# Kernel optimization log

Hardware: AMD Instinct MI355X
Metric: run time of the kernel (lower is better)

Reference implementation:

```python
import jax, jax.numpy as jnp
import numpy as np

N = 100000      # nodes
E = 1600000     # edges (avg degree 16)
IN = 128        # input_dim
HID = 32        # hidden_dim per head (layer 1)
HEADS = 2       # heads (layer 1)
OUT = 32        # output_dim (layer 2, heads=1)
NEG_SLOPE = 0.2 # PyG GATConv default leaky relu slope


def setup_inputs() -> dict:
    key = jax.random.key(0)
    ks = jax.random.split(key, 10)
    s = 0.1  # glorot-ish scale
    x = jax.random.normal(ks[0], (N, IN), jnp.float32)
    edge_index = jax.random.randint(ks[1], (2, E), 0, N, dtype=jnp.int64)
    W1 = jax.random.normal(ks[2], (IN, HEADS * HID), jnp.float32) * s
    a1_src = jax.random.normal(ks[3], (HEADS, HID), jnp.float32) * s
    a1_dst = jax.random.normal(ks[4], (HEADS, HID), jnp.float32) * s
    b1 = jnp.zeros((HEADS * HID,), jnp.float32)
    W2 = jax.random.normal(ks[5], (HEADS * HID, OUT), jnp.float32) * s
    a2_src = jax.random.normal(ks[6], (1, OUT), jnp.float32) * s
    a2_dst = jax.random.normal(ks[7], (1, OUT), jnp.float32) * s
    b2 = jnp.zeros((OUT,), jnp.float32)
    return {"x": x, "edge_index": edge_index, "W1": W1, "a1_src": a1_src,
            "a1_dst": a1_dst, "b1": b1, "W2": W2, "a2_src": a2_src,
            "a2_dst": a2_dst, "b2": b2}


def _gat_layer(x, src, dst, W, a_src, a_dst, b, heads, out_ch, concat, n_nodes):
    # linear projection: [N, heads, out_ch]
    h = (x @ W).reshape(n_nodes, heads, out_ch)
    # per-node attention halves: [N, heads]
    alpha_s = jnp.einsum('nhc,hc->nh', h, a_src)
    alpha_d = jnp.einsum('nhc,hc->nh', h, a_dst)
    # per-edge raw score (message x_j = source node, softmax over dst segment)
    e = jax.nn.leaky_relu(alpha_s[src] + alpha_d[dst], NEG_SLOPE)  # [E, heads]
    # segment softmax over incoming edges of each dst node
    m = jax.ops.segment_max(e, dst, num_segments=n_nodes)          # [N, heads]
    m = jax.lax.stop_gradient(m)
    ee = jnp.exp(e - m[dst])
    denom = jax.ops.segment_sum(ee, dst, num_segments=n_nodes)     # [N, heads]
    alpha = ee / (denom[dst] + 1e-16)                              # [E, heads]
    # weighted scatter-add aggregation
    msg = h[src] * alpha[:, :, None]                               # [E, heads, out_ch]
    out = jax.ops.segment_sum(msg, dst, num_segments=n_nodes)      # [N, heads, out_ch]
    if concat:
        out = out.reshape(n_nodes, heads * out_ch)
    else:
        out = out.mean(axis=1)
    return out + b


def reference(x, edge_index, W1, a1_src, a1_dst, b1, W2, a2_src, a2_dst, b2):
    n = x.shape[0]
    # PyG GATConv adds self-loops by default (both layers, same edge set)
    loop = jnp.arange(n, dtype=edge_index.dtype)
    src = jnp.concatenate([edge_index[0], loop])
    dst = jnp.concatenate([edge_index[1], loop])
    h = _gat_layer(x, src, dst, W1, a1_src, a1_dst, b1, HEADS, HID, True, n)
    h = jax.nn.elu(h)
    return _gat_layer(h, src, dst, W2, a2_src, a2_dst, b2, 1, OUT, False, n)
```

## Files before the change

kernel.cpp:

```cpp
#include <hip/hip_runtime.h>
#include <math.h>

#define N_NODES 100000
#define N_EDGES 1600000
#define IN_DIM  128
#define C1      64
#define OUT_DIM 32
#define NEG_SLOPE 0.2f
#define LOG2E 1.44269504f

#define BSHIFT  8
#define BNODES  256
#define NBUCK   ((N_NODES + BNODES - 1) / BNODES)
#define CAP     5120
#define SLOTS   48
#define GC_STRIDE 16
#define G1_BLOCKS ((N_NODES + 127) / 128)
#define B1_BLOCKS ((N_EDGES + 4095) / 4096)

typedef _Float16 half8 __attribute__((ext_vector_type(8)));
typedef float    f32x4 __attribute__((ext_vector_type(4)));

__device__ __forceinline__ float wexp2(float sc) {
    return __builtin_amdgcn_exp2f(fmaxf(sc, NEG_SLOPE * sc));
}

__global__ void prep_k(const float* __restrict__ W1, const float* __restrict__ W2,
                       _Float16* __restrict__ w1t, _Float16* __restrict__ w2t,
                       int* __restrict__ gcur) {
    int t = blockIdx.x * 256 + threadIdx.x;
    if (t < NBUCK * GC_STRIDE) gcur[t] = 0;
    if (t < IN_DIM * C1) {
        int k = t >> 6, n = t & 63;
        w1t[n * IN_DIM + k] = (_Float16)W1[t];
    }
    if (t < C1 * OUT_DIM) {
        int k = t >> 5, n = t & 31;
        w2t[n * C1 + k] = (_Float16)W2[t];
    }
}

__global__ __launch_bounds__(256) void b1g1_k(const int* __restrict__ ei,
        int* __restrict__ gcur, int* __restrict__ buf,
        const float* __restrict__ x, const _Float16* __restrict__ w1t,
        const float* __restrict__ a_s, const float* __restrict__ a_d,
        _Float16* __restrict__ h, float* __restrict__ as_o,
        float* __restrict__ ad_o) {
    __shared__ __align__(16) char smem[4 * 32 * 72 * 2];
    int t = threadIdx.x;

    if (blockIdx.x < B1_BLOCKS) {
        int* scnt  = (int*)smem;
        int* sbase = scnt + NBUCK;
        int* soff  = sbase + NBUCK;
        for (int i = t; i < NBUCK; i += 256) { scnt[i] = 0; soff[i] = 0; }
        __syncthreads();
        int  s[16], bk[16], ld[16];
        bool v[16];
        #pragma unroll
        for (int i = 0; i < 16; ++i) {
            int e = blockIdx.x * 4096 + i * 256 + t;
            v[i] = e < N_EDGES;
            int ec = v[i] ? e : 0;
            s[i] = ei[ec];
            int d = ei[N_EDGES + ec];
            bk[i] = d >> BSHIFT;
            ld[i] = d & (BNODES - 1);
            if (v[i]) atomicAdd(&scnt[bk[i]], 1);
        }
        __syncthreads();
        for (int i = t; i < NBUCK; i += 256)
            sbase[i] = scnt[i] ? atomicAdd(&gcur[i * GC_STRIDE], scnt[i]) : 0;
        __syncthreads();
        #pragma unroll
        for (int i = 0; i < 16; ++i) {
            if (v[i]) {
                int p = sbase[bk[i]] + atomicAdd(&soff[bk[i]], 1);
                if (p < CAP) buf[bk[i] * CAP + p] = s[i] | (ld[i] << 17);
            }
        }
        return;
    }

    _Float16 (*sh)[32 * 72] = (_Float16(*)[32 * 72])smem;
    int wv = t >> 6, lane = t & 63, m = lane & 15, q = lane >> 4;
    int rbw = (blockIdx.x - B1_BLOCKS) * 128 + wv * 32;
    f32x4 acc[2][4];
    #pragma unroll
    for (int i = 0; i < 2; ++i)
        #pragma unroll
        for (int j = 0; j < 4; ++j) acc[i][j] = (f32x4){0.f, 0.f, 0.f, 0.f};
    #pragma unroll
    for (int ks = 0; ks < 4; ++ks) {
        half8 a[2];
        #pragma unroll
        for (int rt = 0; rt < 2; ++rt) {
            int r = rbw + rt * 16 + m;
            r = r < N_NODES ? r : 0;
            const float4* p = (const float4*)(x + (size_t)r * IN_DIM + ks * 32 + q * 8);
            float4 f0 = p[0], f1 = p[1];
            half8 av;
            av[0] = (_Float16)f0.x; av[1] = (_Float16)f0.y;
            av[2] = (_Float16)f0.z; av[3] = (_Float16)f0.w;
            av[4] = (_Float16)f1.x; av[5] = (_Float16)f1.y;
            av[6] = (_Float16)f1.z; av[7] = (_Float16)f1.w;
            a[rt] = av;
        }
        #pragma unroll
        for (int ct = 0; ct < 4; ++ct) {
            half8 b = *(const half8*)(w1t + (ct * 16 + m) * IN_DIM + ks * 32 + q * 8);
            acc[0][ct] = __builtin_amdgcn_mfma_f32_16x16x32_f16(a[0], b, acc[0][ct], 0, 0, 0);
            acc[1][ct] = __builtin_amdgcn_mfma_f32_16x16x32_f16(a[1], b, acc[1][ct], 0, 0, 0);
        }
    }
    _Float16* ws = sh[wv];
    #pragma unroll
    for (int rt = 0; rt < 2; ++rt)
        #pragma unroll
        for (int ct = 0; ct < 4; ++ct)
            #pragma unroll
            for (int r = 0; r < 4; ++r)
                ws[(rt * 16 + q * 4 + r) * 72 + ct * 16 + m] = (_Float16)acc[rt][ct][r];
    __syncthreads();
    int rl = lane >> 1, hp = lane & 1;
    int rg = rbw + rl;
    if (rg < N_NODES) {
        float As_r[32], Ad_r[32];
        const float4* ap = (const float4*)(a_s + hp * 32);
        const float4* dp = (const float4*)(a_d + hp * 32);
        #pragma unroll
        for (int i = 0; i < 8; ++i) {
            float4 v = ap[i];
            As_r[4*i] = v.x; As_r[4*i+1] = v.y; As_r[4*i+2] = v.z; As_r[4*i+3] = v.w;
            float4 u = dp[i];
            Ad_r[4*i] = u.x; Ad_r[4*i+1] = u.y; Ad_r[4*i+2] = u.z; Ad_r[4*i+3] = u.w;
        }
        const _Float16* rowp = ws + rl * 72 + hp * 32;
        half8 c0 = *(const half8*)(rowp);
        half8 c1 = *(const half8*)(rowp + 8);
        half8 c2 = *(const half8*)(rowp + 16);
        half8 c3 = *(const half8*)(rowp + 24);
        float s = 0.f, dd = 0.f;
        #pragma unroll
        for (int j = 0; j < 8; ++j) {
            s  = fmaf((float)c0[j], As_r[j],      s);
            dd = fmaf((float)c0[j], Ad_r[j],      dd);
            s  = fmaf((float)c1[j], As_r[8 + j],  s);
            dd = fmaf((float)c1[j], Ad_r[8 + j],  dd);
            s  = fmaf((float)c2[j], As_r[16 + j], s);
            dd = fmaf((float)c2[j], Ad_r[16 + j], dd);
            s  = fmaf((float)c3[j], As_r[24 + j], s);
            dd = fmaf((float)c3[j], Ad_r[24 + j], dd);
        }
        as_o[rg * 2 + hp] = s  * LOG2E;
        ad_o[rg * 2 + hp] = dd * LOG2E;
        _Float16* hr = h + (size_t)rg * C1 + hp * 32;
        *(half8*)(hr)      = c0;
        *(half8*)(hr + 8)  = c1;
        *(half8*)(hr + 16) = c2;
        *(half8*)(hr + 24) = c3;
    }
}

__global__ __launch_bounds__(256) void binp2_k(const int* __restrict__ gcur,
        const int* __restrict__ buf, int* __restrict__ csr, int* __restrict__ deg) {
    __shared__ int4 lcsr4[BNODES * SLOTS / 4];
    __shared__ int  lcnt[BNODES];
    int* lcsr = (int*)lcsr4;
    int b = blockIdx.x, t = threadIdx.x;
    lcnt[t] = 0;
    __syncthreads();
    int cnt = gcur[b * GC_STRIDE];
    if (cnt > CAP) cnt = CAP;
    const int* bb = buf + b * CAP;
    for (int e = t; e < cnt; e += 256) {
        int vv = bb[e];
        int src = vv & 0x1FFFF;
        int l = vv >> 17;
        int slot = atomicAdd(&lcnt[l], 1);
        if (slot < SLOTS) lcsr[l * SLOTS + slot] = src;
    }
    __syncthreads();
    int c = lcnt[t];
    int slot = c < SLOTS ? c : SLOTS - 1;
    lcsr[t * SLOTS + slot] = b * BNODES + t;
    int cd = c + 1;
    deg[b * BNODES + t] = cd < SLOTS ? cd : SLOTS;
    __syncthreads();
    int4* g4 = (int4*)csr + (size_t)b * (BNODES * SLOTS / 4);
    #pragma unroll
    for (int i = 0; i < BNODES * SLOTS / 4 / 256; ++i)
        g4[t + i * 256] = lcsr4[t + i * 256];
}

__global__ __launch_bounds__(256) void agg1g2_k(const int* __restrict__ deg,
        const int* __restrict__ csr, const _Float16* __restrict__ h1,
        const float* __restrict__ as1, const float* __restrict__ ad1,
        const float* __restrict__ b1, const _Float16* __restrict__ w2t,
        const float* __restrict__ a2s, const float* __restrict__ a2d,
        _Float16* __restrict__ h2, float* __restrict__ as2o,
        float* __restrict__ ad2o) {
    __shared__ int      srow[16 * SLOTS];
    __shared__ _Float16 shu[16 * 72];
    __shared__ _Float16 sh2[16 * 36];
    int t = threadIdx.x;
    int wv = t >> 6, lane = t & 63;
    int dl   = lane >> 4;
    int eg   = (lane >> 3) & 1;
    int cl   = lane & 7;
    int head = cl >> 2;
    int lr   = wv * 4 + dl;
    int d    = blockIdx.x * 16 + lr;

    if (t < 16 * SLOTS / 4)
        ((int4*)srow)[t] = ((const int4*)(csr + (size_t)blockIdx.x * 16 * SLOTS))[t];
    __syncthreads();

    int cnt = deg[d];
    const int* row = srow + lr * SLOTS;
    float advl = ad1[d * 2 + head];
    float acc[8] = {0.f, 0.f, 0.f, 0.f, 0.f, 0.f, 0.f, 0.f};
    float wsum = 0.f;
    for (int base = 0; base < cnt; base += 8) {
        int e0 = base + eg, e1 = e0 + 2, e2 = e0 + 4, e3 = e0 + 6;
        bool v0 = e0 < cnt, v1 = e1 < cnt, v2 = e2 < cnt, v3 = e3 < cnt;
        int s0 = row[v0 ? e0 : 0];
        int s1 = row[v1 ? e1 : 0];
        int s2 = row[v2 ? e2 : 0];
        int s3 = row[v3 ? e3 : 0];
        float a0 = as1[(unsigned)(s0 * 2 + head)];
        float a1 = as1[(unsigned)(s1 * 2 + head)];
        float a2 = as1[(unsigned)(s2 * 2 + head)];
        float a3 = as1[(unsigned)(s3 * 2 + head)];
        half8 g0 = *(const half8*)(h1 + (unsigned)(s0 * C1 + 8 * cl));
        half8 g1 = *(const half8*)(h1 + (unsigned)(s1 * C1 + 8 * cl));
        half8 g2 = *(const half8*)(h1 + (unsigned)(s2 * C1 + 8 * cl));
        half8 g3 = *(const half8*)(h1 + (unsigned)(s3 * C1 + 8 * cl));
        float w0 = v0 ? wexp2(a0 + advl) : 0.f;
        float w1 = v1 ? wexp2(a1 + advl) : 0.f;
        float w2 = v2 ? wexp2(a2 + advl) : 0.f;
        float w3 = v3 ? wexp2(a3 + advl) : 0.f;
        #pragma unroll
        for (int i = 0; i < 8; ++i) {
            acc[i] = fmaf((float)g0[i], w0, acc[i]);
            acc[i] = fmaf((float)g1[i], w1, acc[i]);
            acc[i] = fmaf((float)g2[i], w2, acc[i]);
            acc[i] = fmaf((float)g3[i], w3, acc[i]);
        }
        wsum += (w0 + w1) + (w2 + w3);
    }
    #pragma unroll
    for (int i = 0; i < 8; ++i) acc[i] += __shfl_xor(acc[i], 8);
    wsum += __shfl_xor(wsum, 8);
    if (eg == 0) {
        float inv = 1.f / (wsum + 1e-16f);
        const float4* bv = (const float4*)(b1 + 8 * cl);
        float o[8];
        #pragma unroll
        for (int i = 0; i < 4; ++i) {
            o[i]     = acc[i]     * inv + (&bv[0].x)[i];
            o[4 + i] = acc[4 + i] * inv + (&bv[1].x)[i];
        }
        half8 hv;
        #pragma unroll
        for (int i = 0; i < 8; ++i) {
            float e = o[i] > 0.f ? o[i] : __expf(o[i]) - 1.f;
            hv[i] = (_Float16)e;
        }
        *(half8*)(shu + lr * 72 + cl * 8) = hv;
    }
    __syncthreads();
    if (wv != 0) return;

    {
        int m = lane & 15, q = lane >> 4;
        f32x4 c2[2];
        c2[0] = (f32x4){0.f, 0.f, 0.f, 0.f};
        c2[1] = (f32x4){0.f, 0.f, 0.f, 0.f};
        #pragma unroll
        for (int ks = 0; ks < 2; ++ks) {
            half8 a = *(const half8*)(shu + m * 72 + ks * 32 + q * 8);
            #pragma unroll
            for (int ct = 0; ct < 2; ++ct) {
                half8 b = *(const half8*)(w2t + (ct * 16 + m) * C1 + ks * 32 + q * 8);
                c2[ct] = __builtin_amdgcn_mfma_f32_16x16x32_f16(a, b, c2[ct], 0, 0, 0);
            }
        }
        #pragma unroll
        for (int ct = 0; ct < 2; ++ct)
            #pragma unroll
            for (int r = 0; r < 4; ++r)
                sh2[(q * 4 + r) * 36 + ct * 16 + m] = (_Float16)c2[ct][r];
    }
    asm volatile("s_waitcnt lgkmcnt(0)" ::: "memory");
    __builtin_amdgcn_sched_barrier(0);

    {
        int r = lane & 15, p = lane >> 4;
        int rg = blockIdx.x * 16 + r;
        const float4* ap = (const float4*)(a2s + p * 8);
        const float4* dp = (const float4*)(a2d + p * 8);
        float4 av0 = ap[0], av1 = ap[1];
        float4 dv0 = dp[0], dv1 = dp[1];
        float As[8] = {av0.x, av0.y, av0.z, av0.w, av1.x, av1.y, av1.z, av1.w};
        float Ad[8] = {dv0.x, dv0.y, dv0.z, dv0.w, dv1.x, dv1.y, dv1.z, dv1.w};
        half8 c = *(const half8*)(sh2 + r * 36 + p * 8);
        float s = 0.f, dd = 0.f;
        #pragma unroll
        for (int j = 0; j < 8; ++j) {
            s  = fmaf((float)c[j], As[j], s);
            dd = fmaf((float)c[j], Ad[j], dd);
        }
        s  += __shfl_xor(s, 16);  s  += __shfl_xor(s, 32);
        dd += __shfl_xor(dd, 16); dd += __shfl_xor(dd, 32);
        if (p == 0) {
            as2o[rg] = s  * LOG2E;
            ad2o[rg] = dd * LOG2E;
        }
        *(half8*)(h2 + (size_t)rg * OUT_DIM + p * 8) = c;
    }
}

__global__ __launch_bounds__(256) void agg2_k(const int* __restrict__ deg,
        const int* __restrict__ csr, const _Float16* __restrict__ h2,
        const float* __restrict__ as2, const float* __restrict__ ad2,
        const float* __restrict__ b2, float* __restrict__ out) {
    __shared__ int srow[32 * SLOTS];
    int t = threadIdx.x;
    int wv = t >> 6, lane = t & 63;
    int dl   = lane >> 3;
    int eg   = (lane >> 2) & 1;
    int cl   = lane & 3;
    int lr   = wv * 8 + dl;
    int d    = blockIdx.x * 32 + lr;

    {
        int4* s4 = (int4*)srow;
        const int4* g4 = (const int4*)(csr + (size_t)blockIdx.x * 32 * SLOTS);
        s4[t] = g4[t];
        if (t < 128) s4[256 + t] = g4[256 + t];
    }
    __syncthreads();

    int cnt = deg[d];
    const int* row = srow + lr * SLOTS;
    float advl = ad2[d];
    float acc[8] = {0.f, 0.f, 0.f, 0.f, 0.f, 0.f, 0.f, 0.f};
    float wsum = 0.f;
    for (int base = 0; base < cnt; base += 8) {
        int e0 = base + eg, e1 = e0 + 2, e2 = e0 + 4, e3 = e0 + 6;
        bool v0 = e0 < cnt, v1 = e1 < cnt, v2 = e2 < cnt, v3 = e3 < cnt;
        int s0 = row[v0 ? e0 : 0];
        int s1 = row[v1 ? e1 : 0];
        int s2 = row[v2 ? e2 : 0];
        int s3 = row[v3 ? e3 : 0];
        float a0 = as2[(unsigned)s0];
        float a1 = as2[(unsigned)s1];
        float a2 = as2[(unsigned)s2];
        float a3 = as2[(unsigned)s3];
        half8 g0 = *(const half8*)(h2 + (unsigned)(s0 * OUT_DIM + 8 * cl));
        half8 g1 = *(const half8*)(h2 + (unsigned)(s1 * OUT_DIM + 8 * cl));
        half8 g2 = *(const half8*)(h2 + (unsigned)(s2 * OUT_DIM + 8 * cl));
        half8 g3 = *(const half8*)(h2 + (unsigned)(s3 * OUT_DIM + 8 * cl));
        float w0 = v0 ? wexp2(a0 + advl) : 0.f;
        float w1 = v1 ? wexp2(a1 + advl) : 0.f;
        float w2 = v2 ? wexp2(a2 + advl) : 0.f;
        float w3 = v3 ? wexp2(a3 + advl) : 0.f;
        #pragma unroll
        for (int i = 0; i < 8; ++i) {
            acc[i] = fmaf((float)g0[i], w0, acc[i]);
            acc[i] = fmaf((float)g1[i], w1, acc[i]);
            acc[i] = fmaf((float)g2[i], w2, acc[i]);
            acc[i] = fmaf((float)g3[i], w3, acc[i]);
        }
        wsum += (w0 + w1) + (w2 + w3);
    }
    #pragma unroll
    for (int i = 0; i < 8; ++i) acc[i] += __shfl_xor(acc[i], 4);
    wsum += __shfl_xor(wsum, 4);
    if (eg == 0) {
        float inv = 1.f / (wsum + 1e-16f);
        const float4* bv = (const float4*)(b2 + 8 * cl);
        float4 o0, o1;
        o0.x = acc[0] * inv + bv[0].x; o0.y = acc[1] * inv + bv[0].y;
        o0.z = acc[2] * inv + bv[0].z; o0.w = acc[3] * inv + bv[0].w;
        o1.x = acc[4] * inv + bv[1].x; o1.y = acc[5] * inv + bv[1].y;
        o1.z = acc[6] * inv + bv[1].z; o1.w = acc[7] * inv + bv[1].w;
        float4* ow = (float4*)(out + (size_t)d * OUT_DIM + 8 * cl);
        ow[0] = o0;
        ow[1] = o1;
    }
}


extern "C" void kernel_launch(void* const* d_in, const int* in_sizes, int n_in,
                              void* d_out, int out_size, void* d_ws, size_t ws_size,
                              hipStream_t stream) {
    const float* x   = (const float*)d_in[0];
    const int*   ei  = (const int*)d_in[1];
    const float* W1  = (const float*)d_in[2];
    const float* a1s = (const float*)d_in[3];
    const float* a1d = (const float*)d_in[4];
    const float* b1  = (const float*)d_in[5];
    const float* W2  = (const float*)d_in[6];
    const float* a2s = (const float*)d_in[7];
    const float* a2d = (const float*)d_in[8];
    const float* b2  = (const float*)d_in[9];
    float* out = (float*)d_out;

    char* ws = (char*)d_ws;
    size_t off = 0;
    auto alloc = [&](size_t bytes) -> void* {
        void* p = ws + off;
        off = (off + bytes + 255) & ~(size_t)255;
        return p;
    };
    int* gcur      = (int*)alloc((size_t)NBUCK * GC_STRIDE * 4);
    int* buf       = (int*)alloc((size_t)NBUCK * CAP * 4);
    int* csr       = (int*)alloc((size_t)NBUCK * BNODES * SLOTS * 4);
    int* deg       = (int*)alloc((size_t)NBUCK * BNODES * 4);
    _Float16* w1t  = (_Float16*)alloc((size_t)IN_DIM * C1 * 2);
    _Float16* w2t  = (_Float16*)alloc((size_t)C1 * OUT_DIM * 2);
    _Float16* h1   = (_Float16*)alloc((size_t)N_NODES * C1 * 2);
    float* as1     = (float*)alloc((size_t)N_NODES * 2 * 4);
    float* ad1     = (float*)alloc((size_t)N_NODES * 2 * 4);
    _Float16* h2   = (_Float16*)alloc((size_t)N_NODES * OUT_DIM * 2);
    float* as2     = (float*)alloc((size_t)N_NODES * 4);
    float* ad2     = (float*)alloc((size_t)N_NODES * 4);

    prep_k<<<(IN_DIM * C1 + 255) / 256, 256, 0, stream>>>(W1, W2, w1t, w2t, gcur);
    b1g1_k<<<B1_BLOCKS + G1_BLOCKS, 256, 0, stream>>>(ei, gcur, buf,
                                                      x, w1t, a1s, a1d, h1, as1, ad1);
    binp2_k<<<NBUCK, 256, 0, stream>>>(gcur, buf, csr, deg);
    agg1g2_k<<<N_NODES / 16, 256, 0, stream>>>(deg, csr, h1, as1, ad1, b1,
                                               w2t, a2s, a2d, h2, as2, ad2);
    agg2_k<<<N_NODES / 32, 256, 0, stream>>>(deg, csr, h2, as2, ad2, b2, out);
}
```

Measured before the change: 205.3 us.

## Build fixed-slot CSR directly with global atomics, drop two-pass bucket binning

Replaces the two-stage bucketed edge binning (shared-memory bucket counts, global bucket buffer, then a separate per-bucket kernel building the slot CSR) with a single pass where each edge does a global atomicAdd on its destination degree and writes its source straight into the fixed-slot CSR. The self-loop entry is now inserted by the aggregation kernels after they load the row into shared memory. This removes one kernel launch and the intermediate buffer round trip. In exchange it issues roughly 1.6M random global atomics and scattered 4-byte writes, and edge order within each row becomes nondeterministic.

Measured after the change: 275.8 us. +34.3%, slower.

```diff
diff --git a/kernel.cpp b/kernel.cpp
--- a/kernel.cpp
+++ b/kernel.cpp
@@ -9,14 +9,9 @@
 #define NEG_SLOPE 0.2f
 #define LOG2E 1.44269504f
 
-#define BSHIFT  8
-#define BNODES  256
-#define NBUCK   ((N_NODES + BNODES - 1) / BNODES)
-#define CAP     5120
 #define SLOTS   48
-#define GC_STRIDE 16
+#define B1_BLOCKS ((N_EDGES + 2047) / 2048)
 #define G1_BLOCKS ((N_NODES + 127) / 128)
-#define B1_BLOCKS ((N_EDGES + 4095) / 4096)
 
 typedef _Float16 half8 __attribute__((ext_vector_type(8)));
 typedef float    f32x4 __attribute__((ext_vector_type(4)));
@@ -27,9 +22,9 @@
 
 __global__ void prep_k(const float* __restrict__ W1, const float* __restrict__ W2,
                        _Float16* __restrict__ w1t, _Float16* __restrict__ w2t,
-                       int* __restrict__ gcur) {
+                       int* __restrict__ deg) {
     int t = blockIdx.x * 256 + threadIdx.x;
-    if (t < NBUCK * GC_STRIDE) gcur[t] = 0;
+    if (t < N_NODES) deg[t] = 0;
     if (t < IN_DIM * C1) {
         int k = t >> 6, n = t & 63;
         w1t[n * IN_DIM + k] = (_Float16)W1[t];
@@ -41,48 +36,28 @@
 }
 
 __global__ __launch_bounds__(256) void b1g1_k(const int* __restrict__ ei,
-        int* __restrict__ gcur, int* __restrict__ buf,
+        int* __restrict__ deg, int* __restrict__ csr,
         const float* __restrict__ x, const _Float16* __restrict__ w1t,
         const float* __restrict__ a_s, const float* __restrict__ a_d,
         _Float16* __restrict__ h, float* __restrict__ as_o,
         float* __restrict__ ad_o) {
-    __shared__ __align__(16) char smem[4 * 32 * 72 * 2];
+    __shared__ _Float16 sh[4][32 * 72];
     int t = threadIdx.x;
 
     if (blockIdx.x < B1_BLOCKS) {
-        int* scnt  = (int*)smem;
-        int* sbase = scnt + NBUCK;
-        int* soff  = sbase + NBUCK;
-        for (int i = t; i < NBUCK; i += 256) { scnt[i] = 0; soff[i] = 0; }
-        __syncthreads();
-        int  s[16], bk[16], ld[16];
-        bool v[16];
-        #pragma unroll
-        for (int i = 0; i < 16; ++i) {
-            int e = blockIdx.x * 4096 + i * 256 + t;
-            v[i] = e < N_EDGES;
-            int ec = v[i] ? e : 0;
-            s[i] = ei[ec];
-            int d = ei[N_EDGES + ec];
-            bk[i] = d >> BSHIFT;
-            ld[i] = d & (BNODES - 1);
-            if (v[i]) atomicAdd(&scnt[bk[i]], 1);
-        }
-        __syncthreads();
-        for (int i = t; i < NBUCK; i += 256)
-            sbase[i] = scnt[i] ? atomicAdd(&gcur[i * GC_STRIDE], scnt[i]) : 0;
-        __syncthreads();
-        #pragma unroll
-        for (int i = 0; i < 16; ++i) {
-            if (v[i]) {
-                int p = sbase[bk[i]] + atomicAdd(&soff[bk[i]], 1);
-                if (p < CAP) buf[bk[i] * CAP + p] = s[i] | (ld[i] << 17);
+        #pragma unroll
+        for (int i = 0; i < 8; ++i) {
+            int e = blockIdx.x * 2048 + i * 256 + t;
+            if (e < N_EDGES) {
+                int s = ei[e];
+                int d = ei[N_EDGES + e];
+                int slot = atomicAdd(&deg[d], 1);
+                if (slot < SLOTS) csr[d * SLOTS + slot] = s;
             }
         }
         return;
     }
 
-    _Float16 (*sh)[32 * 72] = (_Float16(*)[32 * 72])smem;
     int wv = t >> 6, lane = t & 63, m = lane & 15, q = lane >> 4;
     int rbw = (blockIdx.x - B1_BLOCKS) * 128 + wv * 32;
     f32x4 acc[2][4];
@@ -160,37 +135,6 @@
         *(half8*)(hr + 16) = c2;
         *(half8*)(hr + 24) = c3;
     }
-}
-
-__global__ __launch_bounds__(256) void binp2_k(const int* __restrict__ gcur,
-        const int* __restrict__ buf, int* __restrict__ csr, int* __restrict__ deg) {
-    __shared__ int4 lcsr4[BNODES * SLOTS / 4];
-    __shared__ int  lcnt[BNODES];
-    int* lcsr = (int*)lcsr4;
-    int b = blockIdx.x, t = threadIdx.x;
-    lcnt[t] = 0;
-    __syncthreads();
-    int cnt = gcur[b * GC_STRIDE];
-    if (cnt > CAP) cnt = CAP;
-    const int* bb = buf + b * CAP;
-    for (int e = t; e < cnt; e += 256) {
-        int vv = bb[e];
-        int src = vv & 0x1FFFF;
-        int l = vv >> 17;
-        int slot = atomicAdd(&lcnt[l], 1);
-        if (slot < SLOTS) lcsr[l * SLOTS + slot] = src;
-    }
-    __syncthreads();
-    int c = lcnt[t];
-    int slot = c < SLOTS ? c : SLOTS - 1;
-    lcsr[t * SLOTS + slot] = b * BNODES + t;
-    int cd = c + 1;
-    deg[b * BNODES + t] = cd < SLOTS ? cd : SLOTS;
-    __syncthreads();
-    int4* g4 = (int4*)csr + (size_t)b * (BNODES * SLOTS / 4);
-    #pragma unroll
-    for (int i = 0; i < BNODES * SLOTS / 4 / 256; ++i)
-        g4[t + i * 256] = lcsr4[t + i * 256];
 }
 
 __global__ __launch_bounds__(256) void agg1g2_k(const int* __restrict__ deg,
@@ -215,8 +159,15 @@
     if (t < 16 * SLOTS / 4)
         ((int4*)srow)[t] = ((const int4*)(csr + (size_t)blockIdx.x * 16 * SLOTS))[t];
     __syncthreads();
-
-    int cnt = deg[d];
+    if (t < 16) {
+        int c = deg[blockIdx.x * 16 + t];
+        int sl = c < SLOTS ? c : SLOTS - 1;
+        srow[t * SLOTS + sl] = blockIdx.x * 16 + t;
+    }
+    __syncthreads();
+
+    int craw = deg[d];
+    int cnt = (craw + 1) < SLOTS ? craw + 1 : SLOTS;
     const int* row = srow + lr * SLOTS;
     float advl = ad1[d * 2 + head];
     float acc[8] = {0.f, 0.f, 0.f, 0.f, 0.f, 0.f, 0.f, 0.f};
@@ -341,8 +292,15 @@
         if (t < 128) s4[256 + t] = g4[256 + t];
     }
     __syncthreads();
-
-    int cnt = deg[d];
+    if (t < 32) {
+        int c = deg[blockIdx.x * 32 + t];
+        int sl = c < SLOTS ? c : SLOTS - 1;
+        srow[t * SLOTS + sl] = blockIdx.x * 32 + t;
+    }
+    __syncthreads();
+
+    int craw = deg[d];
+    int cnt = (craw + 1) < SLOTS ? craw + 1 : SLOTS;
     const int* row = srow + lr * SLOTS;
     float advl = ad2[d];
     float acc[8] = {0.f, 0.f, 0.f, 0.f, 0.f, 0.f, 0.f, 0.f};
@@ -415,10 +373,8 @@
         off = (off + bytes + 255) & ~(size_t)255;
         return p;
     };
-    int* gcur      = (int*)alloc((size_t)NBUCK * GC_STRIDE * 4);
-    int* buf       = (int*)alloc((size_t)NBUCK * CAP * 4);
-    int* csr       = (int*)alloc((size_t)NBUCK * BNODES * SLOTS * 4);
-    int* deg       = (int*)alloc((size_t)NBUCK * BNODES * 4);
+    int* csr       = (int*)alloc((size_t)N_NODES * SLOTS * 4);
+    int* deg       = (int*)alloc((size_t)N_NODES * 4);
     _Float16* w1t  = (_Float16*)alloc((size_t)IN_DIM * C1 * 2);
     _Float16* w2t  = (_Float16*)alloc((size_t)C1 * OUT_DIM * 2);
     _Float16* h1   = (_Float16*)alloc((size_t)N_NODES * C1 * 2);
@@ -428,10 +384,9 @@
     float* as2     = (float*)alloc((size_t)N_NODES * 4);
     float* ad2     = (float*)alloc((size_t)N_NODES * 4);
 
-    prep_k<<<(IN_DIM * C1 + 255) / 256, 256, 0, stream>>>(W1, W2, w1t, w2t, gcur);
-    b1g1_k<<<B1_BLOCKS + G1_BLOCKS, 256, 0, stream>>>(ei, gcur, buf,
+    prep_k<<<(N_NODES + 255) / 256, 256, 0, stream>>>(W1, W2, w1t, w2t, deg);
+    b1g1_k<<<B1_BLOCKS + G1_BLOCKS, 256, 0, stream>>>(ei, deg, csr,
                                                       x, w1t, a1s, a1d, h1, as1, ad1);
-    binp2_k<<<NBUCK, 256, 0, stream>>>(gcur, buf, csr, deg);
     agg1g2_k<<<N_NODES / 16, 256, 0, stream>>>(deg, csr, h1, as1, ad1, b1,
                                                w2t, a2s, a2d, h2, as2, ad2);
     agg2_k<<<N_NODES / 32, 256, 0, stream>>>(deg, csr, h2, as2, ad2, b2, out);
```

## Locally sort edges by bucket in LDS before coalesced global scatter

Applied to the files above, without the earlier changes.

The edge-bucketing phase now records each edge's local rank from the first atomic, prefix-scans the per-bucket counts in shared memory, and writes edges into a bucket-sorted LDS staging array. It then writes that array to global buffers with consecutive threads hitting consecutive slots, which replaces the second round of LDS atomics and the scattered global writes with more contiguous stores. In exchange it adds a 9-step block scan with barriers and uses more shared memory, which may lower occupancy for the fused GEMM blocks.

Measured after the change: 201.3 us (median of 2 runs). 1.02x faster.

```diff
diff --git a/kernel.cpp b/kernel.cpp
--- a/kernel.cpp
+++ b/kernel.cpp
@@ -46,37 +46,74 @@
         const float* __restrict__ a_s, const float* __restrict__ a_d,
         _Float16* __restrict__ h, float* __restrict__ as_o,
         float* __restrict__ ad_o) {
-    __shared__ __align__(16) char smem[4 * 32 * 72 * 2];
+    __shared__ __align__(16) char smem[29312];
     int t = threadIdx.x;
 
     if (blockIdx.x < B1_BLOCKS) {
-        int* scnt  = (int*)smem;
-        int* sbase = scnt + NBUCK;
-        int* soff  = sbase + NBUCK;
-        for (int i = t; i < NBUCK; i += 256) { scnt[i] = 0; soff[i] = 0; }
+        int*            ledge = (int*)smem;
+        unsigned short* lbkt  = (unsigned short*)(smem + 16384);
+        int*            scnt  = (int*)(smem + 24576);
+        int*            lbase = scnt + NBUCK;
+        int*            sbase = lbase + NBUCK;
+        for (int i = t; i < NBUCK; i += 256) scnt[i] = 0;
         __syncthreads();
-        int  s[16], bk[16], ld[16];
+        int pk[16], bk[16], p[16];
         bool v[16];
         #pragma unroll
         for (int i = 0; i < 16; ++i) {
             int e = blockIdx.x * 4096 + i * 256 + t;
             v[i] = e < N_EDGES;
             int ec = v[i] ? e : 0;
-            s[i] = ei[ec];
+            int s = ei[ec];
             int d = ei[N_EDGES + ec];
             bk[i] = d >> BSHIFT;
-            ld[i] = d & (BNODES - 1);
-            if (v[i]) atomicAdd(&scnt[bk[i]], 1);
+            pk[i] = s | ((d & (BNODES - 1)) << 17);
+            p[i] = v[i] ? atomicAdd(&scnt[bk[i]], 1) : 0;
         }
         __syncthreads();
-        for (int i = t; i < NBUCK; i += 256)
-            sbase[i] = scnt[i] ? atomicAdd(&gcur[i * GC_STRIDE], scnt[i]) : 0;
+        int* sA = ledge;
+        int* sB = ledge + 512;
+        sA[t]       = t < NBUCK ? scnt[t] : 0;
+        sA[t + 256] = (t + 256) < NBUCK ? scnt[t + 256] : 0;
+        __syncthreads();
+        int* pin = sA; int* pout = sB;
+        for (int off = 1; off < 512; off <<= 1) {
+            pout[t] = pin[t] + (t >= off ? pin[t - off] : 0);
+            int k = t + 256;
+            pout[k] = pin[k] + (k >= off ? pin[k - off] : 0);
+            __syncthreads();
+            int* tmp = pin; pin = pout; pout = tmp;
+        }
+        if (t < NBUCK) {
+            lbase[t] = pin[t] - scnt[t];
+            sbase[t] = scnt[t] ? atomicAdd(&gcur[t * GC_STRIDE], scnt[t]) : 0;
+        }
+        {
+            int k = t + 256;
+            if (k < NBUCK) {
+                lbase[k] = pin[k] - scnt[k];
+                sbase[k] = scnt[k] ? atomicAdd(&gcur[k * GC_STRIDE], scnt[k]) : 0;
+            }
+        }
         __syncthreads();
         #pragma unroll
         for (int i = 0; i < 16; ++i) {
             if (v[i]) {
-                int p = sbase[bk[i]] + atomicAdd(&soff[bk[i]], 1);
-                if (p < CAP) buf[bk[i] * CAP + p] = s[i] | (ld[i] << 17);
+                int slot = lbase[bk[i]] + p[i];
+                ledge[slot] = pk[i];
+                lbkt[slot] = (unsigned short)bk[i];
+            }
+        }
+        __syncthreads();
+        int Eb = N_EDGES - blockIdx.x * 4096;
+        if (Eb > 4096) Eb = 4096;
+        #pragma unroll
+        for (int j = 0; j < 16; ++j) {
+            int slot = j * 256 + t;
+            if (slot < Eb) {
+                int b = lbkt[slot];
+                int pos = sbase[b] + (slot - lbase[b]);
+                if (pos < CAP) buf[b * CAP + pos] = ledge[slot];
             }
         }
         return;
```
